# Performance work log

Measured on AMD Instinct MI355X. Metric: run time of the kernel, lower is better.

## Reference

```python
import jax, jax.numpy as jnp
import numpy as np

B, R, C, NH = 8, 64, 256, 8
N = R * R            # 4096 tokens
HD = C // NH         # head dim 32
FF = 3               # focusing factor

def dwconv(x, w, b):
    # x: (B, C, H, W); w: (C, 1, kh, kw) depthwise
    y = jax.lax.conv_general_dilated(
        x, w, window_strides=(1, 1), padding='SAME',
        dimension_numbers=('NCHW', 'OIHW', 'NCHW'),
        feature_group_count=x.shape[1])
    return y + b[None, :, None, None]

def setup_inputs() -> dict:
    key = jax.random.key(0)
    ks = jax.random.split(key, 6)
    return {
        'qkv': jax.random.normal(ks[0], (3, B, N, C), jnp.float32),
        'pos_enc': jax.random.normal(ks[1], (1, N, C), jnp.float32) * 0.02,
        'scale': jax.random.normal(ks[2], (1, 1, C), jnp.float32) * 0.02,
        'w_v': jax.random.normal(ks[3], (C, 1, 3, 3), jnp.float32) * 0.1,
        'b_v': jnp.zeros((C,), jnp.float32),
        'w_dwc': jax.random.normal(ks[4], (HD, 1, 5, 5), jnp.float32) * 0.1,
        'b_dwc': jnp.zeros((HD,), jnp.float32),
    }

def reference(qkv, pos_enc, scale, w_v, b_v, w_dwc, b_dwc):
    q, k, v = qkv[0], qkv[1], qkv[2]          # each (B, N, C)
    # --- LePE: depthwise 3x3 conv on v over full channel dim ---
    v_img = v.transpose(0, 2, 1).reshape(B, C, R, R)
    lepe = dwconv(v_img, w_v, b_v)            # (B, C, R, R)
    lepe = lepe.reshape(B * NH, HD, N).transpose(0, 2, 1)   # (B*h, N, hd)
    v = v_img.reshape(B, C, N).transpose(0, 2, 1)           # (B, N, C)
    # --- focused kernelization ---
    k = k + pos_enc
    sc = jax.nn.softplus(scale)
    q = (jax.nn.relu(q) + 1e-6) / sc
    k = (jax.nn.relu(k) + 1e-6) / sc
    qn = jnp.linalg.norm(q, axis=-1, keepdims=True)
    kn = jnp.linalg.norm(k, axis=-1, keepdims=True)
    q = q ** FF
    k = k ** FF
    q = q / jnp.linalg.norm(q, axis=-1, keepdims=True) * qn
    k = k / jnp.linalg.norm(k, axis=-1, keepdims=True) * kn
    split = lambda x: x.reshape(B, N, NH, HD).transpose(0, 2, 1, 3).reshape(B * NH, N, HD)
    q, k, v = split(q), split(k), split(v)    # (B*h, N, hd)
    # --- linear attention (kv aggregation path: N >> hd) ---
    z = 1.0 / (jnp.einsum('bic,bc->bi', q, k.sum(axis=1)) + 1e-6)
    kv = jnp.einsum('bjc,bjd->bcd', k, v)     # (B*h, hd, hd)
    x = jnp.einsum('bic,bcd,bi->bid', q, kv, z)
    # --- dwc feature mixing on v per head ---
    fm = v.transpose(0, 2, 1).reshape(B * NH, HD, R, R)
    fm = dwconv(fm, w_dwc, b_dwc).reshape(B * NH, HD, N).transpose(0, 2, 1)
    x = x + fm + lepe
    x = x.reshape(B, NH, N, HD).transpose(0, 2, 1, 3).reshape(B, N, C)
    return x
```

## Files before the change

kernel.cpp:

```cpp
#include <hip/hip_runtime.h>
#include <math.h>

#define B_  8
#define R_  64
#define C_  256
#define NH_ 8
#define N_  4096
#define HD_ 32
#define LDP 260

__device__ __forceinline__ float softplus_rcp(float s) {
    return 1.f / __logf(1.f + __expf(s));
}

__global__ __launch_bounds__(256) void kernelNB5(
        const float* __restrict__ qkv, const float* __restrict__ pos,
        const float* __restrict__ scale,
        float* __restrict__ qs_arr, float* __restrict__ part,
        float* __restrict__ kspart) {
    __shared__ float smem[8576];
    float* rsc_s = smem + 8320;

    const int t    = threadIdx.x;
    const int wave = t >> 6, lane = t & 63;
    const int tk   = lane >> 5;
    const int lr   = lane & 31;
    const int blk  = blockIdx.x;
    const int tok0 = blk * 64;
    const int row  = wave * 2 + tk;

    rsc_s[t] = softplus_rcp(scale[t]);

    const size_t qbase = (size_t)tok0 * C_;
    const size_t koff  = (size_t)B_ * N_ * C_;
    const size_t voff  = (size_t)2 * B_ * N_ * C_;

    const int h  = t >> 5;
    const int l  = t & 31;
    const int cg = l & 7;
    const int dg = l >> 3;

    float acc[4][8];
    #pragma unroll
    for (int ii = 0; ii < 4; ii++)
        #pragma unroll
        for (int jj = 0; jj < 8; jj++) acc[ii][jj] = 0.f;
    float ksp[4] = {0.f, 0.f, 0.f, 0.f};

    float4 sq[2], sk[2], sv[2], sp[2];
    float  rs[8];

    auto LOAD = [&](int tt) {
        const int    nrow = tt * 8 + row;
        const size_t off  = qbase + (size_t)nrow * C_;
        const size_t poff = (size_t)((tok0 + nrow) & (N_ - 1)) * C_;
        #pragma unroll
        for (int j = 0; j < 2; j++) {
            const int c = j * 128 + lr * 4;
            sq[j] = *(const float4*)(qkv + off + c);
            sk[j] = *(const float4*)(qkv + koff + off + c);
            sv[j] = *(const float4*)(qkv + voff + off + c);
            sp[j] = *(const float4*)(pos + poff + c);
        }
    };

    auto PROC = [&](int tt) {
        float* kf_s = (tt & 1) ? smem + 2080 : smem;
        float* v_s  = (tt & 1) ? smem + 6240 : smem + 4160;
        const int tok = tok0 + tt * 8 + row;
        float kc[8];
        float sq2 = 0.f, sq6 = 0.f, sk2 = 0.f, sk6 = 0.f;
        #pragma unroll
        for (int j = 0; j < 2; j++) {
            const int c = j * 128 + lr * 4;
            *(float4*)&v_s[row * LDP + c] = sv[j];
            const float qa[4] = {sq[j].x, sq[j].y, sq[j].z, sq[j].w};
            const float ka[4] = {sk[j].x, sk[j].y, sk[j].z, sk[j].w};
            const float pa[4] = {sp[j].x, sp[j].y, sp[j].z, sp[j].w};
            #pragma unroll
            for (int e = 0; e < 4; e++) {
                const float r  = rs[j * 4 + e];
                const float qv = (fmaxf(qa[e], 0.f) + 1e-6f) * r;
                const float kw = (fmaxf(ka[e] + pa[e], 0.f) + 1e-6f) * r;
                sq2 += qv * qv;  sk2 += kw * kw;
                const float q3 = qv * qv * qv, k3 = kw * kw * kw;
                sq6 += q3 * q3;  sk6 += k3 * k3;
                kc[j * 4 + e] = k3;
            }
        }
        #pragma unroll
        for (int m = 1; m < 32; m <<= 1) {
            sq2 += __shfl_xor(sq2, m, 64);
            sq6 += __shfl_xor(sq6, m, 64);
            sk2 += __shfl_xor(sk2, m, 64);
            sk6 += __shfl_xor(sk6, m, 64);
        }
        if (lr == 0) qs_arr[tok] = sqrtf(sq2) * rsqrtf(sq6);
        const float ks = sqrtf(sk2) * rsqrtf(sk6);
        #pragma unroll
        for (int j = 0; j < 2; j++) {
            const float4 kf4 = make_float4(kc[j*4+0] * ks, kc[j*4+1] * ks,
                                           kc[j*4+2] * ks, kc[j*4+3] * ks);
            *(float4*)&kf_s[row * LDP + j * 128 + lr * 4] = kf4;
        }
    };

    auto COMP = [&](int tt) {
        const float* kf_s = (tt & 1) ? smem + 2080 : smem;
        const float* v_s  = (tt & 1) ? smem + 6240 : smem + 4160;
        const float* kfp = kf_s + h * HD_ + cg * 4;
        const float* vp  = v_s  + h * HD_ + dg * 8;
        #pragma unroll
        for (int nl = 0; nl < 8; nl++) {
            const float4 kr = *(const float4*)(kfp + nl * LDP);
            const float4 va = *(const float4*)(vp  + nl * LDP);
            const float4 vb = *(const float4*)(vp  + nl * LDP + 4);
            ksp[0] += kr.x;  ksp[1] += kr.y;
            ksp[2] += kr.z;  ksp[3] += kr.w;
            const float kk[4] = {kr.x, kr.y, kr.z, kr.w};
            const float vv[8] = {va.x, va.y, va.z, va.w,
                                 vb.x, vb.y, vb.z, vb.w};
            #pragma unroll
            for (int ii = 0; ii < 4; ii++)
                #pragma unroll
                for (int jj = 0; jj < 8; jj++)
                    acc[ii][jj] = fmaf(kk[ii], vv[jj], acc[ii][jj]);
        }
    };

    LOAD(0);
    __syncthreads();
    #pragma unroll
    for (int j = 0; j < 2; j++)
        *(float4*)&rs[j * 4] = *(const float4*)&rsc_s[j * 128 + lr * 4];
    PROC(0);
    LOAD(1);
    __syncthreads();
    #pragma unroll
    for (int tt = 0; tt < 8; tt++) {
        COMP(tt);
        if (tt < 7) PROC(tt + 1);
        if (tt < 6) LOAD(tt + 2);
        if (tt < 7) __syncthreads();
    }
    __syncthreads();

    #pragma unroll
    for (int ii = 0; ii < 4; ii++) {
        const float4 a = make_float4(acc[ii][0], acc[ii][1], acc[ii][2], acc[ii][3]);
        const float4 b = make_float4(acc[ii][4], acc[ii][5], acc[ii][6], acc[ii][7]);
        const int base = h * 1024 + (cg * 4 + ii) * 32 + dg * 8;
        *(float4*)&smem[base]     = a;
        *(float4*)&smem[base + 4] = b;
    }
    if (dg == 0)
        *(float4*)&kspart[(size_t)blk * 256 + h * 32 + cg * 4] =
            make_float4(ksp[0], ksp[1], ksp[2], ksp[3]);
    __syncthreads();
    float* pdst = part + (size_t)blk * 8192;
    #pragma unroll
    for (int i = 0; i < 8; i++)
        *(float4*)&pdst[i * 1024 + t * 4] = *(const float4*)&smem[i * 1024 + t * 4];
}

__global__ __launch_bounds__(256) void kernelR(
        const float* __restrict__ part, const float* __restrict__ kspart,
        float* __restrict__ kv_ws, float* __restrict__ ksum_ws) {
    const int t  = threadIdx.x;
    const int bh = blockIdx.x >> 2, q = blockIdx.x & 3;
    const int b  = bh >> 3, h = bh & 7;

    const float* p = part + (size_t)(b * 64) * 8192 + h * 1024 + q * 256 + t;
    float s = 0.f;
    #pragma unroll 4
    for (int j = 0; j < 64; j++) s += p[(size_t)j * 8192];
    kv_ws[bh * 1024 + q * 256 + t] = s;

    if (q == 0 && t < 32) {
        const float* kp = kspart + (size_t)(b * 64) * 256 + h * 32 + t;
        float s2 = 0.f;
        #pragma unroll 8
        for (int j = 0; j < 64; j++) s2 += kp[(size_t)j * 256];
        ksum_ws[bh * 32 + t] = s2;
    }
}

__global__ __launch_bounds__(256) void kernelCD3(
        const float* __restrict__ qkv, const float* __restrict__ qs_arr,
        const float* __restrict__ kv_ws, const float* __restrict__ ksum_ws,
        const float* __restrict__ scale,
        const float* __restrict__ w_v,  const float* __restrict__ b_v,
        const float* __restrict__ w_dwc, const float* __restrict__ b_dwc,
        float* __restrict__ out) {
    __shared__ float v_s[20 * 20 * 32];
    __shared__ float rsc_s[32];
    const int t    = threadIdx.x;
    const int tile = blockIdx.x;
    const int h    = blockIdx.y;
    const int b    = blockIdx.z;
    const int ty0  = (tile >> 2) * 16, tx0 = (tile & 3) * 16;
    const int bh   = b * NH_ + h;

    const float4 kvr = ((const float4*)(kv_ws + (size_t)bh * 1024))[t];
    float ksr = 0.f;
    if (t < 32) {
        ksr      = ksum_ws[bh * HD_ + t];
        rsc_s[t] = softplus_rcp(scale[h * HD_ + t]);
    }

    const float* vb = qkv + (size_t)2 * B_ * N_ * C_ + (size_t)b * N_ * C_ + h * HD_;
    #pragma unroll
    for (int i = 0; i < 13; i++) {
        const int idx = i * 256 + t;
        if (idx < 3200) {
            const int pix = idx >> 3, d4 = (idx & 7) * 4;
            const int yy = pix / 20, xx = pix - yy * 20;
            const int gy = ty0 + yy - 2, gx = tx0 + xx - 2;
            float4 val = make_float4(0.f, 0.f, 0.f, 0.f);
            if (gy >= 0 && gy < R_ && gx >= 0 && gx < R_)
                val = *(const float4*)(vb + (size_t)(gy * R_ + gx) * C_ + d4);
            *(float4*)&v_s[pix * 32 + d4] = val;
        }
    }

    const int c  = t & 31, pg = t >> 5;
    float wv[9], wd[25];
    {
        const float* wvp = w_v + (size_t)(h * HD_ + c) * 9;
        const float* wdp = w_dwc + (size_t)c * 25;
        #pragma unroll
        for (int i = 0; i < 9; i++)  wv[i] = wvp[i];
        #pragma unroll
        for (int i = 0; i < 25; i++) wd[i] = wdp[i];
    }
    const float bias = b_v[h * HD_ + c] + b_dwc[c];
    __syncthreads();

    float res[32];
    #pragma unroll
    for (int r2 = 0; r2 < 2; r2++) {
        const int ty = pg * 2 + r2;
        float win[5][5];
        #pragma unroll
        for (int j = 0; j < 5; j++)
            #pragma unroll
            for (int i = 0; i < 5; i++)
                win[j][i] = v_s[((ty + i) * 20 + j) * 32 + c];
        #pragma unroll
        for (int tx = 0; tx < 16; tx++) {
            float a = bias;
            #pragma unroll
            for (int j = 0; j < 5; j++) {
                const int slot = (tx + j) % 5;
                #pragma unroll
                for (int i = 0; i < 5; i++)
                    a = fmaf(wd[i * 5 + j], win[slot][i], a);
            }
            #pragma unroll
            for (int j = 1; j < 4; j++) {
                const int slot = (tx + j) % 5;
                #pragma unroll
                for (int i = 1; i < 4; i++)
                    a = fmaf(wv[(i - 1) * 3 + (j - 1)], win[slot][i], a);
            }
            res[r2 * 16 + tx] = a;
            if (tx < 15) {
                const int slot = tx % 5;
                #pragma unroll
                for (int i = 0; i < 5; i++)
                    win[slot][i] = v_s[((ty + i) * 20 + (tx + 5)) * 32 + c];
            }
        }
    }
    __syncthreads();
    #pragma unroll
    for (int r2 = 0; r2 < 2; r2++)
        #pragma unroll
        for (int tx = 0; tx < 16; tx++)
            v_s[((pg * 2 + r2) * 16 + tx) * 33 + c] = res[r2 * 16 + tx];
    *(float4*)&v_s[8448 + t * 4] = kvr;
    if (t < 32) v_s[9472 + t] = ksr;
    __syncthreads();

    {
        const int tyy = t >> 4, txx = t & 15;
        const int n   = (ty0 + tyy) * R_ + (tx0 + txx);
        const int tok = b * N_ + n;
        float q[32];
        const float4* qsrc = (const float4*)(qkv + (size_t)tok * C_ + h * HD_);
        #pragma unroll
        for (int i = 0; i < 8; i++) ((float4*)q)[i] = qsrc[i];
        const float qs = qs_arr[tok];
        #pragma unroll
        for (int i = 0; i < 32; i++) {
            const float r = (fmaxf(q[i], 0.f) + 1e-6f) * rsc_s[i];
            q[i] = r * r * r * qs;
        }

        float denom = 1e-6f;
        #pragma unroll
        for (int cc = 0; cc < 32; cc++) denom = fmaf(q[cc], v_s[9472 + cc], denom);
        const float z = 1.f / denom;

        float o[32];
        #pragma unroll
        for (int i = 0; i < 32; i++) o[i] = 0.f;
        #pragma unroll
        for (int cc = 0; cc < 32; cc++) {
            const float qc = q[cc];
            #pragma unroll
            for (int d = 0; d < 32; d++)
                o[d] = fmaf(qc, v_s[8448 + cc * 32 + d], o[d]);
        }
        float4* dst = (float4*)(out + (size_t)tok * C_ + h * HD_);
        #pragma unroll
        for (int i = 0; i < 8; i++) {
            float4 v4;
            v4.x = fmaf(o[i*4+0], z, v_s[t * 33 + i*4+0]);
            v4.y = fmaf(o[i*4+1], z, v_s[t * 33 + i*4+1]);
            v4.z = fmaf(o[i*4+2], z, v_s[t * 33 + i*4+2]);
            v4.w = fmaf(o[i*4+3], z, v_s[t * 33 + i*4+3]);
            dst[i] = v4;
        }
    }
}

extern "C" void kernel_launch(void* const* d_in, const int* in_sizes, int n_in,
                              void* d_out, int out_size, void* d_ws, size_t ws_size,
                              hipStream_t stream) {
    const float* qkv   = (const float*)d_in[0];
    const float* pos   = (const float*)d_in[1];
    const float* scale = (const float*)d_in[2];
    const float* w_v   = (const float*)d_in[3];
    const float* b_v   = (const float*)d_in[4];
    const float* w_dwc = (const float*)d_in[5];
    const float* b_dwc = (const float*)d_in[6];
    float* out = (float*)d_out;

    float* qs_arr  = (float*)d_ws;
    float* part    = qs_arr + (size_t)B_ * N_;
    float* kspart  = part + (size_t)512 * 8192;
    float* kv_ws   = kspart + (size_t)512 * 256;
    float* ksum_ws = kv_ws + 64 * 1024;

    kernelNB5<<<dim3(512), 256, 0, stream>>>(qkv, pos, scale, qs_arr, part, kspart);
    kernelR<<<dim3(256), 256, 0, stream>>>(part, kspart, kv_ws, ksum_ws);
    kernelCD3<<<dim3(16, NH_, B_), 256, 0, stream>>>(qkv, qs_arr, kv_ws, ksum_ws,
                                                     scale, w_v, b_v, w_dwc, b_dwc, out);
}
```

Baseline: 225.8 us.

## Load V directly into LDS via global_load_lds and halve tokens per block

The k-v aggregation kernel now copies V straight from global memory into shared memory with the AMD global_load_lds builtin instead of going through registers. The padded row stride is dropped. The pipeline barrier is moved before the next prefetch so the asynchronous writes do not race with reads of the previous buffer. Each block now handles 32 tokens instead of 64, doubling the grid to 1024 blocks with occupancy hints, and the reduction kernel sums twice as many partials. This trades more partial-sum traffic and reduction work for more parallelism and fewer register round-trips, and the unpadded layout may bring LDS bank conflicts.

```diff
diff --git a/kernel.cpp b/kernel.cpp
--- a/kernel.cpp
+++ b/kernel.cpp
@@ -7,26 +7,31 @@
 #define NH_ 8
 #define N_  4096
 #define HD_ 32
-#define LDP 260
 
 __device__ __forceinline__ float softplus_rcp(float s) {
     return 1.f / __logf(1.f + __expf(s));
 }
 
-__global__ __launch_bounds__(256) void kernelNB5(
+__device__ __forceinline__ void gload16_lds(const float* g, float* l) {
+    __builtin_amdgcn_global_load_lds(
+        (const __attribute__((address_space(1))) unsigned int*)g,
+        (__attribute__((address_space(3))) unsigned int*)l, 16, 0, 0);
+}
+
+__global__ __launch_bounds__(256, 4) void kernelNB6(
         const float* __restrict__ qkv, const float* __restrict__ pos,
         const float* __restrict__ scale,
         float* __restrict__ qs_arr, float* __restrict__ part,
         float* __restrict__ kspart) {
-    __shared__ float smem[8576];
-    float* rsc_s = smem + 8320;
+    __shared__ float smem[8448];
+    float* rsc_s = smem + 8192;
 
     const int t    = threadIdx.x;
     const int wave = t >> 6, lane = t & 63;
     const int tk   = lane >> 5;
     const int lr   = lane & 31;
     const int blk  = blockIdx.x;
-    const int tok0 = blk * 64;
+    const int tok0 = blk * 32;
     const int row  = wave * 2 + tk;
 
     rsc_s[t] = softplus_rcp(scale[t]);
@@ -47,33 +52,33 @@
         for (int jj = 0; jj < 8; jj++) acc[ii][jj] = 0.f;
     float ksp[4] = {0.f, 0.f, 0.f, 0.f};
 
-    float4 sq[2], sk[2], sv[2], sp[2];
+    float4 sq[2], sk[2], sp[2];
     float  rs[8];
 
     auto LOAD = [&](int tt) {
+        float* vdst = smem + 4096 + (tt & 1) * 2048;
+        const int r0 = wave * 2;
+        const size_t vsrc = voff + qbase + (size_t)(tt * 8 + r0) * C_;
+        gload16_lds(qkv + vsrc + lane * 4,      vdst + r0 * 256 + lane * 4);
+        gload16_lds(qkv + vsrc + C_ + lane * 4, vdst + (r0 + 1) * 256 + lane * 4);
         const int    nrow = tt * 8 + row;
         const size_t off  = qbase + (size_t)nrow * C_;
         const size_t poff = (size_t)((tok0 + nrow) & (N_ - 1)) * C_;
-        #pragma unroll
-        for (int j = 0; j < 2; j++) {
-            const int c = j * 128 + lr * 4;
-            sq[j] = *(const float4*)(qkv + off + c);
-            sk[j] = *(const float4*)(qkv + koff + off + c);
-            sv[j] = *(const float4*)(qkv + voff + off + c);
-            sp[j] = *(const float4*)(pos + poff + c);
-        }
+        sq[0] = *(const float4*)(qkv + off + lr * 4);
+        sq[1] = *(const float4*)(qkv + off + 128 + lr * 4);
+        sk[0] = *(const float4*)(qkv + koff + off + lr * 4);
+        sk[1] = *(const float4*)(qkv + koff + off + 128 + lr * 4);
+        sp[0] = *(const float4*)(pos + poff + lr * 4);
+        sp[1] = *(const float4*)(pos + poff + 128 + lr * 4);
     };
 
     auto PROC = [&](int tt) {
-        float* kf_s = (tt & 1) ? smem + 2080 : smem;
-        float* v_s  = (tt & 1) ? smem + 6240 : smem + 4160;
+        float* kf_s = smem + (tt & 1) * 2048;
         const int tok = tok0 + tt * 8 + row;
         float kc[8];
         float sq2 = 0.f, sq6 = 0.f, sk2 = 0.f, sk6 = 0.f;
         #pragma unroll
         for (int j = 0; j < 2; j++) {
-            const int c = j * 128 + lr * 4;
-            *(float4*)&v_s[row * LDP + c] = sv[j];
             const float qa[4] = {sq[j].x, sq[j].y, sq[j].z, sq[j].w};
             const float ka[4] = {sk[j].x, sk[j].y, sk[j].z, sk[j].w};
             const float pa[4] = {sp[j].x, sp[j].y, sp[j].z, sp[j].w};
@@ -101,20 +106,20 @@
         for (int j = 0; j < 2; j++) {
             const float4 kf4 = make_float4(kc[j*4+0] * ks, kc[j*4+1] * ks,
                                            kc[j*4+2] * ks, kc[j*4+3] * ks);
-            *(float4*)&kf_s[row * LDP + j * 128 + lr * 4] = kf4;
+            *(float4*)&kf_s[row * 256 + j * 128 + lr * 4] = kf4;
         }
     };
 
     auto COMP = [&](int tt) {
-        const float* kf_s = (tt & 1) ? smem + 2080 : smem;
-        const float* v_s  = (tt & 1) ? smem + 6240 : smem + 4160;
+        const float* kf_s = smem + (tt & 1) * 2048;
+        const float* v_s  = smem + 4096 + (tt & 1) * 2048;
         const float* kfp = kf_s + h * HD_ + cg * 4;
         const float* vp  = v_s  + h * HD_ + dg * 8;
         #pragma unroll
         for (int nl = 0; nl < 8; nl++) {
-            const float4 kr = *(const float4*)(kfp + nl * LDP);
-            const float4 va = *(const float4*)(vp  + nl * LDP);
-            const float4 vb = *(const float4*)(vp  + nl * LDP + 4);
+            const float4 kr = *(const float4*)(kfp + nl * 256);
+            const float4 va = *(const float4*)(vp  + nl * 256);
+            const float4 vb = *(const float4*)(vp  + nl * 256 + 4);
             ksp[0] += kr.x;  ksp[1] += kr.y;
             ksp[2] += kr.z;  ksp[3] += kr.w;
             const float kk[4] = {kr.x, kr.y, kr.z, kr.w};
@@ -137,13 +142,12 @@
     LOAD(1);
     __syncthreads();
     #pragma unroll
-    for (int tt = 0; tt < 8; tt++) {
+    for (int tt = 0; tt < 4; tt++) {
         COMP(tt);
-        if (tt < 7) PROC(tt + 1);
-        if (tt < 6) LOAD(tt + 2);
-        if (tt < 7) __syncthreads();
-    }
-    __syncthreads();
+        if (tt < 3) PROC(tt + 1);
+        __syncthreads();
+        if (tt < 2) LOAD(tt + 2);
+    }
 
     #pragma unroll
     for (int ii = 0; ii < 4; ii++) {
@@ -170,22 +174,22 @@
     const int bh = blockIdx.x >> 2, q = blockIdx.x & 3;
     const int b  = bh >> 3, h = bh & 7;
 
-    const float* p = part + (size_t)(b * 64) * 8192 + h * 1024 + q * 256 + t;
+    const float* p = part + (size_t)(b * 128) * 8192 + h * 1024 + q * 256 + t;
     float s = 0.f;
     #pragma unroll 4
-    for (int j = 0; j < 64; j++) s += p[(size_t)j * 8192];
+    for (int j = 0; j < 128; j++) s += p[(size_t)j * 8192];
     kv_ws[bh * 1024 + q * 256 + t] = s;
 
     if (q == 0 && t < 32) {
-        const float* kp = kspart + (size_t)(b * 64) * 256 + h * 32 + t;
+        const float* kp = kspart + (size_t)(b * 128) * 256 + h * 32 + t;
         float s2 = 0.f;
         #pragma unroll 8
-        for (int j = 0; j < 64; j++) s2 += kp[(size_t)j * 256];
+        for (int j = 0; j < 128; j++) s2 += kp[(size_t)j * 256];
         ksum_ws[bh * 32 + t] = s2;
     }
 }
 
-__global__ __launch_bounds__(256) void kernelCD3(
+__global__ __launch_bounds__(256, 3) void kernelCD3(
         const float* __restrict__ qkv, const float* __restrict__ qs_arr,
         const float* __restrict__ kv_ws, const float* __restrict__ ksum_ws,
         const float* __restrict__ scale,
@@ -339,11 +343,11 @@
 
     float* qs_arr  = (float*)d_ws;
     float* part    = qs_arr + (size_t)B_ * N_;
-    float* kspart  = part + (size_t)512 * 8192;
-    float* kv_ws   = kspart + (size_t)512 * 256;
+    float* kspart  = part + (size_t)1024 * 8192;
+    float* kv_ws   = kspart + (size_t)1024 * 256;
     float* ksum_ws = kv_ws + 64 * 1024;
 
-    kernelNB5<<<dim3(512), 256, 0, stream>>>(qkv, pos, scale, qs_arr, part, kspart);
+    kernelNB6<<<dim3(1024), 256, 0, stream>>>(qkv, pos, scale, qs_arr, part, kspart);
     kernelR<<<dim3(256), 256, 0, stream>>>(part, kspart, kv_ws, ksum_ws);
     kernelCD3<<<dim3(16, NH_, B_), 256, 0, stream>>>(qkv, qs_arr, kv_ws, ksum_ws,
                                                      scale, w_v, b_v, w_dwc, b_dwc, out);
```

Result: slower. 291.3 us (+29.0%).
